# Kernel optimization log

Measured on AMD Instinct MI355X. Metric: run time of the kernel, lower is better.

The kernel has to match this reference:

```python
import jax, jax.numpy as jnp
import numpy as np

N_NODES = 50000
N_EDGES = 800000


def _spmm(edge_row, edge_col, edge_w, h):
    # sparse adj @ h via gather + segment-sum: adj[r,c] = edge_w
    msgs = edge_w[:, None] * h[edge_col]          # [E, D] gather
    return jax.ops.segment_sum(msgs, edge_row, num_segments=N_NODES)


def setup_inputs() -> dict:
    key = jax.random.key(0)
    ks = jax.random.split(key, 8)
    x = jax.random.normal(ks[0], (N_NODES, 256), dtype=jnp.float32)
    edge_row = jax.random.randint(ks[1], (N_EDGES,), 0, N_NODES, dtype=jnp.int32)
    edge_col = jax.random.randint(ks[2], (N_EDGES,), 0, N_NODES, dtype=jnp.int32)
    edge_w = jax.random.uniform(ks[3], (N_EDGES,), dtype=jnp.float32)
    W1 = jax.random.normal(ks[4], (256, 128), dtype=jnp.float32) * 0.06
    b1 = jnp.zeros((128,), dtype=jnp.float32)
    W2 = jax.random.normal(ks[5], (128, 32), dtype=jnp.float32) * 0.09
    b2 = jnp.zeros((32,), dtype=jnp.float32)
    return {"x": x, "edge_row": edge_row, "edge_col": edge_col,
            "edge_w": edge_w, "W1": W1, "b1": b1, "W2": W2, "b2": b2}


def reference(x, edge_row, edge_col, edge_w, W1, b1, W2, b2):
    # Layer 1: support = X @ W1 ; out = relu(A @ support + b1)
    # (dropout is identity in eval mode)
    h = jax.nn.relu(_spmm(edge_row, edge_col, edge_w, x @ W1) + b1)
    # Layer 2
    out = jax.nn.relu(_spmm(edge_row, edge_col, edge_w, h @ W2) + b2)
    return out
```

## Files before the change

kernel.cpp:

```cpp
#include <hip/hip_runtime.h>

#define N_NODES 50000
#define N_EDGES 800000
#define D0 256
#define D1 128
#define D2 32
#define CAP 64
#define NB 391
#define BCAP 3072
#define EB 8192
#define P1_BLOCKS 98
#define G1_BLOCKS 196

typedef unsigned short u16;
typedef unsigned int   u32;
typedef unsigned long long u64;
typedef __attribute__((ext_vector_type(8))) short bf16x8;
typedef __attribute__((ext_vector_type(4))) float f32x4;

__device__ inline u32 bf16rne(float f) {
    union { float f; u32 u; } c; c.f = f;
    return (c.u + 0x7FFFu + ((c.u >> 16) & 1u)) >> 16;
}
__device__ inline float bfhi(u32 v) {
    union { u32 u; float f; } c; c.u = v & 0xFFFF0000u; return c.f;
}
__device__ inline float bflo(u32 v) {
    union { u32 u; float f; } c; c.u = v << 16; return c.f;
}

__global__ __launch_bounds__(256) void front_kernel(const float* __restrict__ W1,
                                                    u16* __restrict__ Bsw1,
                                                    const float* __restrict__ W2,
                                                    u16* __restrict__ Bsw2) {
    const int bid = blockIdx.x;
    if (bid < 16) {
        const int id = bid * 256 + threadIdx.x;
        const int lane = id & 63;
        const int t    = (id >> 6) & 7;
        const int ks   = id >> 9;
        const int n     = t * 16 + (lane & 15);
        const int kbase = ks * 32 + (lane >> 4) * 8;
        u32 v[8];
        #pragma unroll
        for (int j = 0; j < 8; ++j) v[j] = bf16rne(W1[(kbase + j) * D1 + n]);
        uint4 w;
        w.x = v[0] | (v[1] << 16);
        w.y = v[2] | (v[3] << 16);
        w.z = v[4] | (v[5] << 16);
        w.w = v[6] | (v[7] << 16);
        ((uint4*)Bsw1)[id] = w;
    } else {
        const int id = (bid - 16) * 256 + threadIdx.x;
        const int lane = id & 63;
        const int t    = (id >> 6) & 1;
        const int ks   = id >> 7;
        const int n     = t * 16 + (lane & 15);
        const int kbase = ks * 32 + (lane >> 4) * 8;
        u32 v[8];
        #pragma unroll
        for (int j = 0; j < 8; ++j) v[j] = bf16rne(W2[(kbase + j) * D2 + n]);
        uint4 w;
        w.x = v[0] | (v[1] << 16);
        w.y = v[2] | (v[3] << 16);
        w.z = v[4] | (v[5] << 16);
        w.w = v[6] | (v[7] << 16);
        ((uint4*)Bsw2)[id] = w;
    }
}

__global__ __launch_bounds__(1024) void mid_kernel(const float* __restrict__ x,
                                                   const u16* __restrict__ Bsw1,
                                                   u16* __restrict__ s1b,
                                                   const int* __restrict__ erow,
                                                   const int* __restrict__ ecol,
                                                   const float* __restrict__ ew,
                                                   u32* __restrict__ bcur,
                                                   u64* __restrict__ ebuf) {
    const int bid = blockIdx.x;
    const int tid = threadIdx.x;
    if (bid < P1_BLOCKS) {
        __shared__ u32 hist[NB];
        __shared__ u32 lbase[NB];
        for (int i = tid; i < NB; i += 1024) hist[i] = 0;
        __syncthreads();
        const int ebase = bid * EB;
        #pragma unroll
        for (int k = 0; k < EB / 1024; ++k) {
            const int e = ebase + k * 1024 + tid;
            if (e < N_EDGES) atomicAdd(&hist[erow[e] >> 7], 1u);
        }
        __syncthreads();
        for (int i = tid; i < NB; i += 1024) {
            const u32 h = hist[i];
            lbase[i] = h ? atomicAdd(&bcur[i], h) : 0u;
            hist[i] = 0;
        }
        __syncthreads();
        #pragma unroll
        for (int k = 0; k < EB / 1024; ++k) {
            const int e = ebase + k * 1024 + tid;
            if (e < N_EDGES) {
                const int r = erow[e];
                const int c = ecol[e];
                const float w = ew[e];
                const int b = r >> 7;
                const u32 lr = atomicAdd(&hist[b], 1u);
                const u32 pos = lbase[b] + lr;
                if (pos < BCAP)
                    ebuf[(size_t)b * BCAP + pos] =
                        (u64)(u32)c | ((u64)(u32)(r & 127) << 16) | ((u64)bf16rne(w) << 32);
            }
        }
    } else {
        const int gb   = bid - P1_BLOCKS;
        const int lane = tid & 63;
        const int wave = tid >> 6;
        const int rowbase = gb * 256 + wave * 16;
        const int m    = lane & 15;
        const int quad = lane >> 4;
        int arow = rowbase + m;
        if (arow >= N_NODES) arow = N_NODES - 1;
        const float* aptr = x + (size_t)arow * D0 + quad * 8;

        f32x4 acc[8];
        #pragma unroll
        for (int t = 0; t < 8; ++t) acc[t] = (f32x4){0.f, 0.f, 0.f, 0.f};

        #pragma unroll
        for (int ks = 0; ks < 8; ++ks) {
            const float4 f0 = *(const float4*)(aptr + ks * 32);
            const float4 f1 = *(const float4*)(aptr + ks * 32 + 4);
            bf16x8 a;
            a[0] = (short)bf16rne(f0.x); a[1] = (short)bf16rne(f0.y);
            a[2] = (short)bf16rne(f0.z); a[3] = (short)bf16rne(f0.w);
            a[4] = (short)bf16rne(f1.x); a[5] = (short)bf16rne(f1.y);
            a[6] = (short)bf16rne(f1.z); a[7] = (short)bf16rne(f1.w);
            const u16* bp = Bsw1 + ((size_t)(ks * 8) * 64 + lane) * 8;
            #pragma unroll
            for (int t = 0; t < 8; ++t) {
                const bf16x8 b = *(const bf16x8*)(bp + (size_t)t * 64 * 8);
                acc[t] = __builtin_amdgcn_mfma_f32_16x16x32_bf16(a, b, acc[t], 0, 0, 0);
            }
        }
        const int orow = rowbase + quad * 4;
        #pragma unroll
        for (int r = 0; r < 4; ++r) {
            const int row = orow + r;
            if (row < N_NODES) {
                u16* op = s1b + (size_t)row * D1 + m;
                #pragma unroll
                for (int t = 0; t < 8; ++t) op[t * 16] = (u16)bf16rne(acc[t][r]);
            }
        }
    }
}

__global__ __launch_bounds__(256) void bucket_kernel(const u32* __restrict__ bcur,
                                                     const u64* __restrict__ ebuf,
                                                     int* __restrict__ cnt,
                                                     u32* __restrict__ eg) {
    const int b = blockIdx.x;
    __shared__ u32 seg[128 * CAP];
    __shared__ u32 lcnt[128];
    for (int i = threadIdx.x; i < 128; i += 256) lcnt[i] = 0;
    __syncthreads();
    int n = (int)bcur[b];
    if (n > BCAP) n = BCAP;
    const u64* ep = ebuf + (size_t)b * BCAP;
    for (int i = threadIdx.x; i < n; i += 256) {
        const u64 e = ep[i];
        const u32 c  = (u32)(e & 0xFFFFu);
        const u32 lr = (u32)((e >> 16) & 0x7Fu);
        const u32 w  = (u32)(e >> 32);
        const u32 p = atomicAdd(&lcnt[lr], 1u);
        if (p < CAP)
            seg[lr * CAP + p] = c | (w << 16);
    }
    __syncthreads();
    const int rows = min(128, N_NODES - b * 128);
    for (int i = threadIdx.x; i < rows; i += 256)
        cnt[b * 128 + i] = (int)min(lcnt[i], (u32)CAP);
    u32* dst = eg + (size_t)b * 128 * CAP;
    const int nvec = rows * (CAP / 4);
    for (int i = threadIdx.x; i < nvec; i += 256)
        ((uint4*)dst)[i] = ((const uint4*)seg)[i];
}

__global__ __launch_bounds__(256) void spmm_csr128_kernel(const int* __restrict__ cnt,
                                                          const u32* __restrict__ eg,
                                                          const u16* __restrict__ src,
                                                          const float* __restrict__ bias,
                                                          u16* __restrict__ dst) {
    const int lane = threadIdx.x;
    const int row  = blockIdx.x * 8 + threadIdx.y;
    if (row >= N_NODES) return;
    int len = cnt[row];
    if (len > CAP) len = CAP;
    const u32* ep = eg + (size_t)row * CAP;
    float4 a0 = {0.f,0.f,0.f,0.f}, a1 = {0.f,0.f,0.f,0.f};
    float4 a2 = {0.f,0.f,0.f,0.f}, a3 = {0.f,0.f,0.f,0.f};
    int j = 0;
    for (; j + 3 < len; j += 4) {
        const uint4 e4 = *(const uint4*)(ep + j);
        const uint2 v0 = ((const uint2*)(src + (size_t)(e4.x & 0xFFFFu) * D1))[lane];
        const uint2 v1 = ((const uint2*)(src + (size_t)(e4.y & 0xFFFFu) * D1))[lane];
        const uint2 v2 = ((const uint2*)(src + (size_t)(e4.z & 0xFFFFu) * D1))[lane];
        const uint2 v3 = ((const uint2*)(src + (size_t)(e4.w & 0xFFFFu) * D1))[lane];
        const float w0 = bfhi(e4.x), w1 = bfhi(e4.y), w2 = bfhi(e4.z), w3 = bfhi(e4.w);
        a0.x += w0 * bflo(v0.x); a0.y += w0 * bfhi(v0.x);
        a0.z += w0 * bflo(v0.y); a0.w += w0 * bfhi(v0.y);
        a1.x += w1 * bflo(v1.x); a1.y += w1 * bfhi(v1.x);
        a1.z += w1 * bflo(v1.y); a1.w += w1 * bfhi(v1.y);
        a2.x += w2 * bflo(v2.x); a2.y += w2 * bfhi(v2.x);
        a2.z += w2 * bflo(v2.y); a2.w += w2 * bfhi(v2.y);
        a3.x += w3 * bflo(v3.x); a3.y += w3 * bfhi(v3.x);
        a3.z += w3 * bflo(v3.y); a3.w += w3 * bfhi(v3.y);
    }
    for (; j < len; ++j) {
        const u32 e0 = ep[j];
        const float w0 = bfhi(e0);
        const uint2 v0 = ((const uint2*)(src + (size_t)(e0 & 0xFFFFu) * D1))[lane];
        a0.x += w0 * bflo(v0.x); a0.y += w0 * bfhi(v0.x);
        a0.z += w0 * bflo(v0.y); a0.w += w0 * bfhi(v0.y);
    }
    const float4 b4 = ((const float4*)bias)[lane];
    float rx = a0.x + a1.x + a2.x + a3.x + b4.x; rx = rx > 0.f ? rx : 0.f;
    float ry = a0.y + a1.y + a2.y + a3.y + b4.y; ry = ry > 0.f ? ry : 0.f;
    float rz = a0.z + a1.z + a2.z + a3.z + b4.z; rz = rz > 0.f ? rz : 0.f;
    float rw = a0.w + a1.w + a2.w + a3.w + b4.w; rw = rw > 0.f ? rw : 0.f;
    uint2 o;
    o.x = bf16rne(rx) | (bf16rne(ry) << 16);
    o.y = bf16rne(rz) | (bf16rne(rw) << 16);
    ((uint2*)(dst + (size_t)row * D1))[lane] = o;
}

__global__ __launch_bounds__(256) void gemm2_mfma_kernel(const u16* __restrict__ hb,
                                                         const u16* __restrict__ Bsw2,
                                                         u16* __restrict__ s2b) {
    const int lane = threadIdx.x & 63;
    const int wave = threadIdx.x >> 6;
    const int rowbase = blockIdx.x * 64 + wave * 16;
    const int m    = lane & 15;
    const int quad = lane >> 4;
    int arow = rowbase + m;
    if (arow >= N_NODES) arow = N_NODES - 1;
    const u16* aptr = hb + (size_t)arow * D1 + quad * 8;

    f32x4 acc0 = (f32x4){0.f,0.f,0.f,0.f};
    f32x4 acc1 = (f32x4){0.f,0.f,0.f,0.f};

    #pragma unroll
    for (int ks = 0; ks < 4; ++ks) {
        const bf16x8 a = *(const bf16x8*)(aptr + ks * 32);
        const u16* bp = Bsw2 + ((size_t)(ks * 2) * 64 + lane) * 8;
        const bf16x8 b0 = *(const bf16x8*)(bp);
        const bf16x8 b1 = *(const bf16x8*)(bp + (size_t)64 * 8);
        acc0 = __builtin_amdgcn_mfma_f32_16x16x32_bf16(a, b0, acc0, 0, 0, 0);
        acc1 = __builtin_amdgcn_mfma_f32_16x16x32_bf16(a, b1, acc1, 0, 0, 0);
    }
    const int orow = rowbase + quad * 4;
    #pragma unroll
    for (int r = 0; r < 4; ++r) {
        const int row = orow + r;
        if (row < N_NODES) {
            u16* op = s2b + (size_t)row * D2 + m;
            op[0]  = (u16)bf16rne(acc0[r]);
            op[16] = (u16)bf16rne(acc1[r]);
        }
    }
}

__global__ __launch_bounds__(256) void spmm_csr32_kernel(const int* __restrict__ cnt,
                                                         const u32* __restrict__ eg,
                                                         const u16* __restrict__ src,
                                                         const float* __restrict__ bias,
                                                         float* __restrict__ out) {
    const int lane = threadIdx.x;
    const int row  = blockIdx.x * 16 + threadIdx.y;
    if (row >= N_NODES) return;
    int len = cnt[row];
    if (len > CAP) len = CAP;
    const u32* ep = eg + (size_t)row * CAP;
    float ax0=0.f, ay0=0.f, ax1=0.f, ay1=0.f, ax2=0.f, ay2=0.f, ax3=0.f, ay3=0.f;
    int j = 0;
    for (; j + 3 < len; j += 4) {
        const uint4 e4 = *(const uint4*)(ep + j);
        const u32 v0 = ((const u32*)(src + (size_t)(e4.x & 0xFFFFu) * D2))[lane];
        const u32 v1 = ((const u32*)(src + (size_t)(e4.y & 0xFFFFu) * D2))[lane];
        const u32 v2 = ((const u32*)(src + (size_t)(e4.z & 0xFFFFu) * D2))[lane];
        const u32 v3 = ((const u32*)(src + (size_t)(e4.w & 0xFFFFu) * D2))[lane];
        const float w0 = bfhi(e4.x), w1 = bfhi(e4.y), w2 = bfhi(e4.z), w3 = bfhi(e4.w);
        ax0 += w0 * bflo(v0); ay0 += w0 * bfhi(v0);
        ax1 += w1 * bflo(v1); ay1 += w1 * bfhi(v1);
        ax2 += w2 * bflo(v2); ay2 += w2 * bfhi(v2);
        ax3 += w3 * bflo(v3); ay3 += w3 * bfhi(v3);
    }
    for (; j < len; ++j) {
        const u32 e0 = ep[j];
        const u32 v0 = ((const u32*)(src + (size_t)(e0 & 0xFFFFu) * D2))[lane];
        const float w0 = bfhi(e0);
        ax0 += w0 * bflo(v0); ay0 += w0 * bfhi(v0);
    }
    const float2 b2v = ((const float2*)bias)[lane];
    float vx = ax0 + ax1 + ax2 + ax3 + b2v.x; vx = vx > 0.f ? vx : 0.f;
    float vy = ay0 + ay1 + ay2 + ay3 + b2v.y; vy = vy > 0.f ? vy : 0.f;
    ((float2*)(out + (size_t)row * D2))[lane] = make_float2(vx, vy);
}

extern "C" void kernel_launch(void* const* d_in, const int* in_sizes, int n_in,
                              void* d_out, int out_size, void* d_ws, size_t ws_size,
                              hipStream_t stream) {
    const float* x    = (const float*)d_in[0];
    const int*   erow = (const int*)  d_in[1];
    const int*   ecol = (const int*)  d_in[2];
    const float* ew   = (const float*)d_in[3];
    const float* W1   = (const float*)d_in[4];
    const float* b1   = (const float*)d_in[5];
    const float* W2   = (const float*)d_in[6];
    const float* b2   = (const float*)d_in[7];
    float* out = (float*)d_out;

    int* cnt   = (int*)d_ws;
    u32* bcur  = (u32*)(cnt + N_NODES);
    u32* eg    = (u32*)(bcur + 512);
    u16* Bsw1  = (u16*)(eg + (size_t)N_NODES * CAP);
    u16* Bsw2  = Bsw1 + 8 * 8 * 64 * 8;
    u16* s1b   = Bsw2 + 4 * 2 * 64 * 8;
    u16* hb    = s1b + (size_t)N_NODES * D1;
    u16* s2b   = hb + (size_t)N_NODES * D1;
    u64* ebuf  = (u64*)hb;

    hipMemsetAsync(bcur, 0, 512 * sizeof(u32), stream);
    front_kernel<<<18, 256, 0, stream>>>(W1, Bsw1, W2, Bsw2);
    mid_kernel<<<P1_BLOCKS + G1_BLOCKS, 1024, 0, stream>>>(
        x, Bsw1, s1b, erow, ecol, ew, bcur, ebuf);
    bucket_kernel<<<NB, 256, 0, stream>>>(bcur, ebuf, cnt, eg);
    spmm_csr128_kernel<<<(N_NODES + 7) / 8, dim3(32, 8), 0, stream>>>(cnt, eg, s1b, b1, hb);
    gemm2_mfma_kernel<<<(N_NODES + 63) / 64, 256, 0, stream>>>(hb, Bsw2, s2b);
    spmm_csr32_kernel<<<(N_NODES + 15) / 16, dim3(16, 16), 0, stream>>>(cnt, eg, s2b, b2, out);
}
```

Measured before the change: 204.0 us.

## Move GEMM1 from scatter kernel into bucket kernel as co-scheduled blocks

The edge scatter pass now runs alone in its own kernel, and the dense X@W1 MFMA GEMM now runs in the same launch as the per-bucket CSR build. That launch uses 256-thread blocks, with 64 rows per GEMM block instead of 256. The aim is to overlap the compute-heavy GEMM with the latency-bound bucket pass rather than with the scatter, and to get better block balance from smaller GEMM blocks. The GEMM blocks now carry the bucket kernel's large static shared-memory allocation, which may limit occupancy.

Measured after the change: 195.2 us. 1.05x faster.

```diff
diff --git a/kernel.cpp b/kernel.cpp
--- a/kernel.cpp
+++ b/kernel.cpp
@@ -9,8 +9,8 @@
 #define NB 391
 #define BCAP 3072
 #define EB 8192
-#define P1_BLOCKS 98
-#define G1_BLOCKS 196
+#define SC_BLOCKS 98
+#define G1_BLOCKS 782
 
 typedef unsigned short u16;
 typedef unsigned int   u32;
@@ -69,54 +69,85 @@
     }
 }
 
-__global__ __launch_bounds__(1024) void mid_kernel(const float* __restrict__ x,
-                                                   const u16* __restrict__ Bsw1,
-                                                   u16* __restrict__ s1b,
-                                                   const int* __restrict__ erow,
-                                                   const int* __restrict__ ecol,
-                                                   const float* __restrict__ ew,
-                                                   u32* __restrict__ bcur,
-                                                   u64* __restrict__ ebuf) {
+__global__ __launch_bounds__(1024) void scatter_kernel(const int* __restrict__ erow,
+                                                       const int* __restrict__ ecol,
+                                                       const float* __restrict__ ew,
+                                                       u32* __restrict__ bcur,
+                                                       u64* __restrict__ ebuf) {
+    __shared__ u32 hist[NB];
+    __shared__ u32 lbase[NB];
+    const int tid = threadIdx.x;
+    if (tid < NB) hist[tid] = 0;
+    __syncthreads();
+    const int ebase = blockIdx.x * EB;
+    #pragma unroll
+    for (int k = 0; k < EB / 1024; ++k) {
+        const int e = ebase + k * 1024 + tid;
+        if (e < N_EDGES) atomicAdd(&hist[erow[e] >> 7], 1u);
+    }
+    __syncthreads();
+    if (tid < NB) {
+        const u32 h = hist[tid];
+        lbase[tid] = h ? atomicAdd(&bcur[tid], h) : 0u;
+        hist[tid] = 0;
+    }
+    __syncthreads();
+    #pragma unroll
+    for (int k = 0; k < EB / 1024; ++k) {
+        const int e = ebase + k * 1024 + tid;
+        if (e < N_EDGES) {
+            const int r = erow[e];
+            const int c = ecol[e];
+            const float w = ew[e];
+            const int b = r >> 7;
+            const u32 lr = atomicAdd(&hist[b], 1u);
+            const u32 pos = lbase[b] + lr;
+            if (pos < BCAP)
+                ebuf[(size_t)b * BCAP + pos] =
+                    (u64)(u32)c | ((u64)(u32)(r & 127) << 16) | ((u64)bf16rne(w) << 32);
+        }
+    }
+}
+
+__global__ __launch_bounds__(256) void gb_kernel(const float* __restrict__ x,
+                                                 const u16* __restrict__ Bsw1,
+                                                 u16* __restrict__ s1b,
+                                                 const u32* __restrict__ bcur,
+                                                 const u64* __restrict__ ebuf,
+                                                 int* __restrict__ cnt,
+                                                 u32* __restrict__ eg) {
+    __shared__ u32 seg[128 * CAP];
+    __shared__ u32 lcnt[128];
     const int bid = blockIdx.x;
-    const int tid = threadIdx.x;
-    if (bid < P1_BLOCKS) {
-        __shared__ u32 hist[NB];
-        __shared__ u32 lbase[NB];
-        for (int i = tid; i < NB; i += 1024) hist[i] = 0;
+    if (bid < NB) {
+        const int b = bid;
+        for (int i = threadIdx.x; i < 128; i += 256) lcnt[i] = 0;
         __syncthreads();
-        const int ebase = bid * EB;
-        #pragma unroll
-        for (int k = 0; k < EB / 1024; ++k) {
-            const int e = ebase + k * 1024 + tid;
-            if (e < N_EDGES) atomicAdd(&hist[erow[e] >> 7], 1u);
+        int n = (int)bcur[b];
+        if (n > BCAP) n = BCAP;
+        const u64* ep = ebuf + (size_t)b * BCAP;
+        for (int i = threadIdx.x; i < n; i += 256) {
+            const u64 e = ep[i];
+            const u32 c  = (u32)(e & 0xFFFFu);
+            const u32 lr = (u32)((e >> 16) & 0x7Fu);
+            const u32 w  = (u32)(e >> 32);
+            const u32 p = atomicAdd(&lcnt[lr], 1u);
+            if (p < CAP)
+                seg[lr * CAP + p] = c | (w << 16);
         }
         __syncthreads();
-        for (int i = tid; i < NB; i += 1024) {
-            const u32 h = hist[i];
-            lbase[i] = h ? atomicAdd(&bcur[i], h) : 0u;
-            hist[i] = 0;
-        }
-        __syncthreads();
-        #pragma unroll
-        for (int k = 0; k < EB / 1024; ++k) {
-            const int e = ebase + k * 1024 + tid;
-            if (e < N_EDGES) {
-                const int r = erow[e];
-                const int c = ecol[e];
-                const float w = ew[e];
-                const int b = r >> 7;
-                const u32 lr = atomicAdd(&hist[b], 1u);
-                const u32 pos = lbase[b] + lr;
-                if (pos < BCAP)
-                    ebuf[(size_t)b * BCAP + pos] =
-                        (u64)(u32)c | ((u64)(u32)(r & 127) << 16) | ((u64)bf16rne(w) << 32);
-            }
-        }
+        const int rows = min(128, N_NODES - b * 128);
+        for (int i = threadIdx.x; i < rows; i += 256)
+            cnt[b * 128 + i] = (int)min(lcnt[i], (u32)CAP);
+        u32* dst = eg + (size_t)b * 128 * CAP;
+        const int nvec = rows * (CAP / 4);
+        for (int i = threadIdx.x; i < nvec; i += 256)
+            ((uint4*)dst)[i] = ((const uint4*)seg)[i];
     } else {
-        const int gb   = bid - P1_BLOCKS;
-        const int lane = tid & 63;
-        const int wave = tid >> 6;
-        const int rowbase = gb * 256 + wave * 16;
+        const int gb   = bid - NB;
+        const int lane = threadIdx.x & 63;
+        const int wave = threadIdx.x >> 6;
+        const int rowbase = gb * 64 + wave * 16;
         const int m    = lane & 15;
         const int quad = lane >> 4;
         int arow = rowbase + m;
@@ -154,37 +185,6 @@
             }
         }
     }
-}
-
-__global__ __launch_bounds__(256) void bucket_kernel(const u32* __restrict__ bcur,
-                                                     const u64* __restrict__ ebuf,
-                                                     int* __restrict__ cnt,
-                                                     u32* __restrict__ eg) {
-    const int b = blockIdx.x;
-    __shared__ u32 seg[128 * CAP];
-    __shared__ u32 lcnt[128];
-    for (int i = threadIdx.x; i < 128; i += 256) lcnt[i] = 0;
-    __syncthreads();
-    int n = (int)bcur[b];
-    if (n > BCAP) n = BCAP;
-    const u64* ep = ebuf + (size_t)b * BCAP;
-    for (int i = threadIdx.x; i < n; i += 256) {
-        const u64 e = ep[i];
-        const u32 c  = (u32)(e & 0xFFFFu);
-        const u32 lr = (u32)((e >> 16) & 0x7Fu);
-        const u32 w  = (u32)(e >> 32);
-        const u32 p = atomicAdd(&lcnt[lr], 1u);
-        if (p < CAP)
-            seg[lr * CAP + p] = c | (w << 16);
-    }
-    __syncthreads();
-    const int rows = min(128, N_NODES - b * 128);
-    for (int i = threadIdx.x; i < rows; i += 256)
-        cnt[b * 128 + i] = (int)min(lcnt[i], (u32)CAP);
-    u32* dst = eg + (size_t)b * 128 * CAP;
-    const int nvec = rows * (CAP / 4);
-    for (int i = threadIdx.x; i < nvec; i += 256)
-        ((uint4*)dst)[i] = ((const uint4*)seg)[i];
 }
 
 __global__ __launch_bounds__(256) void spmm_csr128_kernel(const int* __restrict__ cnt,
@@ -333,9 +333,8 @@
 
     hipMemsetAsync(bcur, 0, 512 * sizeof(u32), stream);
     front_kernel<<<18, 256, 0, stream>>>(W1, Bsw1, W2, Bsw2);
-    mid_kernel<<<P1_BLOCKS + G1_BLOCKS, 1024, 0, stream>>>(
-        x, Bsw1, s1b, erow, ecol, ew, bcur, ebuf);
-    bucket_kernel<<<NB, 256, 0, stream>>>(bcur, ebuf, cnt, eg);
+    scatter_kernel<<<SC_BLOCKS, 1024, 0, stream>>>(erow, ecol, ew, bcur, ebuf);
+    gb_kernel<<<NB + G1_BLOCKS, 256, 0, stream>>>(x, Bsw1, s1b, bcur, ebuf, cnt, eg);
     spmm_csr128_kernel<<<(N_NODES + 7) / 8, dim3(32, 8), 0, stream>>>(cnt, eg, s1b, b1, hb);
     gemm2_mfma_kernel<<<(N_NODES + 63) / 64, 256, 0, stream>>>(hb, Bsw2, s2b);
     spmm_csr32_kernel<<<(N_NODES + 15) / 16, dim3(16, 16), 0, stream>>>(cnt, eg, s2b, b2, out);
```
